# Kernel optimization log

Measured on AMD Instinct MI355X. Metric: run time of the kernel, lower is better.

## Reference

```python
import jax, jax.numpy as jnp
import numpy as np

N_NODES = 8192
N_EDGES = 262144
N_REL = 8
NUM_CLASSES = 151
EMB = 256
BOX = 1024
HID = 512
OUT = 256
N_TASKS = 2


def setup_inputs() -> dict:
    key = jax.random.key(0)
    ks = jax.random.split(key, 20)
    w = lambda k, shape: jax.random.normal(k, shape, dtype=jnp.float32) * 0.02
    return {
        "box_features": jax.random.normal(ks[0], (N_NODES, BOX), dtype=jnp.float32),
        "pred_labels": jax.random.randint(ks[1], (N_NODES,), 0, NUM_CLASSES),
        "edge_index": jax.random.randint(ks[2], (2, N_EDGES), 0, N_NODES),
        "edge_type": jax.random.randint(ks[3], (N_EDGES,), 0, N_REL),
        "nodes_per_graph": 128,
        "emb_table": w(ks[4], (NUM_CLASSES, EMB)),
        "W_lin": w(ks[5], (BOX + EMB, HID)),
        "b_lin": jnp.zeros((HID,), jnp.float32),
        "rel_W1": w(ks[6], (N_REL, HID, HID)),
        "root_W1": w(ks[7], (HID, HID)),
        "b1": jnp.zeros((HID,), jnp.float32),
        "rel_W2": w(ks[8], (N_REL, HID, OUT)),
        "root_W2": w(ks[9], (HID, OUT)),
        "b2": jnp.zeros((OUT,), jnp.float32),
        "Wc1": w(ks[10], (OUT, OUT)),
        "bc1": jnp.zeros((OUT,), jnp.float32),
        "Wc2": w(ks[11], (OUT, N_TASKS)),
        "bc2": jnp.zeros((N_TASKS,), jnp.float32),
    }


def rgcn_conv(x, src, dst, etype, rel_W, root_W, b):
    """PyG RGCNConv: per-relation mean aggregation + root weight + bias."""
    R, _, out_dim = rel_W.shape
    N = x.shape[0]
    transformed = jnp.einsum('ni,rio->rno', x, rel_W)      # [R, N, out]
    msg = transformed[etype, src]                           # [E, out] gather per edge
    seg = etype * N + dst                                   # (relation, dst) segment id
    sums = jax.ops.segment_sum(msg, seg, num_segments=R * N)
    cnt = jax.ops.segment_sum(jnp.ones((msg.shape[0],), x.dtype), seg, num_segments=R * N)
    mean = sums / jnp.maximum(cnt, 1.0)[:, None]
    agg = mean.reshape(R, N, out_dim).sum(0)                # sum over relations
    return agg + x @ root_W + b


def reference(box_features, pred_labels, edge_index, edge_type, nodes_per_graph,
              emb_table, W_lin, b_lin, rel_W1, root_W1, b1, rel_W2, root_W2, b2,
              Wc1, bc1, Wc2, bc2):
    src, dst = edge_index[0], edge_index[1]
    # obj embedding + concat with box features
    x = jnp.concatenate([box_features, emb_table[pred_labels]], axis=-1)  # [N, 1280]
    x = x @ W_lin + b_lin                                                  # [N, 512]
    x = jax.nn.relu(rgcn_conv(x, src, dst, edge_type, rel_W1, root_W1, b1))
    x = rgcn_conv(x, src, dst, edge_type, rel_W2, root_W2, b2)             # [N, 256]
    # mean graph pooling over equal-size graphs
    B = x.shape[0] // nodes_per_graph
    pooled = x.reshape(B, nodes_per_graph, -1).mean(axis=1)                # [B, 256]
    # classifier (dropout is identity in eval)
    y_logits = (pooled @ Wc1 + bc1) @ Wc2 + bc2                            # [B, n_tasks]
    y_prob = jax.nn.softmax(y_logits, axis=-1)
    return y_logits, y_prob
```

## Files before the change

kernel.cpp:

```cpp
#include <hip/hip_runtime.h>
#include <cstdint>

#define NNODES 8192
#define NEDGES 262144
#define NRELS  8
#define EMBD   256
#define BOXD   1024
#define HIDD   512
#define OUTD   256
#define NSEG   (NRELS * NNODES)
#define K0DIM  (BOXD + EMBD)
#define KSDIM  (NRELS * HIDD + HIDD)

using bf16x8 = __attribute__((ext_vector_type(8))) short;
using f32x4  = __attribute__((ext_vector_type(4))) float;
using us4    = __attribute__((ext_vector_type(4))) unsigned short;

__device__ __forceinline__ unsigned short f2b(float f) {
    union { float f; uint32_t u; } v; v.f = f;
    uint32_t r = v.u + 0x7FFFu + ((v.u >> 16) & 1u);
    return (unsigned short)(r >> 16);
}

__device__ __forceinline__ us4 cvt4(f32x4 v) {
    us4 u;
    u[0] = f2b(v[0]); u[1] = f2b(v[1]); u[2] = f2b(v[2]); u[3] = f2b(v[3]);
    return u;
}

__device__ __forceinline__ float b2f_lo(uint32_t w) {
    union { uint32_t u; float f; } v; v.u = w << 16; return v.f;
}
__device__ __forceinline__ float b2f_hi(uint32_t w) {
    union { uint32_t u; float f; } v; v.u = w & 0xffff0000u; return v.f;
}

__global__ void k_build_x0(const float* __restrict__ box, const int* __restrict__ labels,
                           const float* __restrict__ emb, unsigned short* __restrict__ X0) {
    int n = blockIdx.x;
    int lab = labels[n];
    const f32x4* b = (const f32x4*)(box + (size_t)n * BOXD);
    const f32x4* e = (const f32x4*)(emb + (size_t)lab * EMBD);
    us4* o = (us4*)(X0 + (size_t)n * K0DIM);
    for (int j = threadIdx.x; j < K0DIM / 4; j += 256) {
        f32x4 v = (j < BOXD / 4) ? b[j] : e[j - BOXD / 4];
        o[j] = cvt4(v);
    }
}

__global__ void k_transpose(const float* __restrict__ src, unsigned short* __restrict__ dst,
                            int No, int ldDst, int kOff) {
    __shared__ float t[32][33];
    int kt = blockIdx.x * 32, ot = blockIdx.y * 32;
    int tx = threadIdx.x & 31, ty = threadIdx.x >> 5;
#pragma unroll
    for (int i = 0; i < 4; i++) {
        int k = kt + ty + i * 8;
        t[ty + i * 8][tx] = src[(size_t)k * No + ot + tx];
    }
    __syncthreads();
#pragma unroll
    for (int i = 0; i < 4; i++) {
        int o = ot + ty + i * 8;
        dst[(size_t)o * ldDst + kOff + kt + tx] = f2b(t[tx][ty + i * 8]);
    }
}

__global__ void k_hist(const int* __restrict__ etype, const int* __restrict__ edst,
                       int* __restrict__ cnt) {
    int e = blockIdx.x * 256 + threadIdx.x;
    if (e >= NEDGES) return;
    atomicAdd(&cnt[etype[e] * NNODES + edst[e]], 1);
}

__global__ void k_scan(const int* __restrict__ cnt, int* __restrict__ segstart) {
    __shared__ int part[256];
    __shared__ int pre[257];
    int t = threadIdx.x;
    int base = t * 256;
    int s = 0;
    for (int i = 0; i < 256; i++) s += cnt[base + i];
    part[t] = s;
    __syncthreads();
    if (t == 0) {
        int a = 0;
        for (int i = 0; i < 256; i++) { pre[i] = a; a += part[i]; }
        pre[256] = a;
    }
    __syncthreads();
    int a = pre[t];
    for (int i = 0; i < 256; i++) { segstart[base + i] = a; a += cnt[base + i]; }
    if (t == 255) segstart[NSEG] = a;
}

__global__ void k_scatter(const int* __restrict__ etype, const int* __restrict__ esrc,
                          const int* __restrict__ edst, const int* __restrict__ segstart,
                          int* __restrict__ cursor, int* __restrict__ esorted) {
    int e = blockIdx.x * 256 + threadIdx.x;
    if (e >= NEDGES) return;
    int key = etype[e] * NNODES + edst[e];
    int pos = atomicAdd(&cursor[key], 1);
    esorted[segstart[key] + pos] = esrc[e];
}

__global__ void k_inv(const int* __restrict__ cnt, float* __restrict__ inv) {
    int s = blockIdx.x * 256 + threadIdx.x;
    if (s >= NSEG) return;
    int c = cnt[s];
    inv[s] = 1.0f / (float)(c > 0 ? c : 1);
}

__global__ __launch_bounds__(256) void k_aggregate(
        const unsigned short* __restrict__ x, const int* __restrict__ segstart,
        const int* __restrict__ esorted, const float* __restrict__ inv,
        unsigned short* __restrict__ Xin) {
    int seg = blockIdx.x * 4 + (threadIdx.x >> 6);
    int lane = threadIdx.x & 63;
    int r = seg >> 13;
    int dstn = seg & (NNODES - 1);
    float a[8] = {0, 0, 0, 0, 0, 0, 0, 0};
    float b[8] = {0, 0, 0, 0, 0, 0, 0, 0};
    int s0 = segstart[seg], s1 = segstart[seg + 1];
    int t = s0;
    for (; t + 2 <= s1; t += 2) {
        uint4 v0 = *(const uint4*)(x + (size_t)esorted[t] * HIDD + lane * 8);
        uint4 v1 = *(const uint4*)(x + (size_t)esorted[t + 1] * HIDD + lane * 8);
        a[0] += b2f_lo(v0.x); a[1] += b2f_hi(v0.x);
        a[2] += b2f_lo(v0.y); a[3] += b2f_hi(v0.y);
        a[4] += b2f_lo(v0.z); a[5] += b2f_hi(v0.z);
        a[6] += b2f_lo(v0.w); a[7] += b2f_hi(v0.w);
        b[0] += b2f_lo(v1.x); b[1] += b2f_hi(v1.x);
        b[2] += b2f_lo(v1.y); b[3] += b2f_hi(v1.y);
        b[4] += b2f_lo(v1.z); b[5] += b2f_hi(v1.z);
        b[6] += b2f_lo(v1.w); b[7] += b2f_hi(v1.w);
    }
    if (t < s1) {
        uint4 v0 = *(const uint4*)(x + (size_t)esorted[t] * HIDD + lane * 8);
        a[0] += b2f_lo(v0.x); a[1] += b2f_hi(v0.x);
        a[2] += b2f_lo(v0.y); a[3] += b2f_hi(v0.y);
        a[4] += b2f_lo(v0.z); a[5] += b2f_hi(v0.z);
        a[6] += b2f_lo(v0.w); a[7] += b2f_hi(v0.w);
    }
    float iv = inv[seg];
#pragma unroll
    for (int j = 0; j < 8; j++) a[j] = (a[j] + b[j]) * iv;
    uint4 u;
    u.x = (uint32_t)f2b(a[0]) | ((uint32_t)f2b(a[1]) << 16);
    u.y = (uint32_t)f2b(a[2]) | ((uint32_t)f2b(a[3]) << 16);
    u.z = (uint32_t)f2b(a[4]) | ((uint32_t)f2b(a[5]) << 16);
    u.w = (uint32_t)f2b(a[6]) | ((uint32_t)f2b(a[7]) << 16);
    *(uint4*)(Xin + (size_t)dstn * KSDIM + r * HIDD + lane * 8) = u;
}

__global__ __launch_bounds__(512, 4) void k_gemm(
        const unsigned short* __restrict__ A,
        const unsigned short* __restrict__ Bt,
        float* __restrict__ P,
        int M, int N, int K, int Kc) {
    __shared__ unsigned short As[2][128 * 64];
    __shared__ unsigned short Bs[2][128 * 64];
    const int tid = threadIdx.x;
    const int lane = tid & 63, wid = tid >> 6;
    const int tiles_m = M >> 7;
    const int tm = blockIdx.x % tiles_m, tn = blockIdx.x / tiles_m;
    const int m0 = tm << 7, n0 = tn << 7;
    const int wr = wid >> 2, wc = wid & 3;
    const int k0 = blockIdx.y * Kc;

    f32x4 acc[4][2];
#pragma unroll
    for (int i = 0; i < 4; i++)
#pragma unroll
        for (int j = 0; j < 2; j++) acc[i][j] = (f32x4){0.f, 0.f, 0.f, 0.f};

    const int rowg = tid >> 3;
    const int srcc = (tid & 7) ^ (rowg & 7);
    const unsigned short* gA = A  + (size_t)(m0 + rowg) * K + k0 + srcc * 8;
    const unsigned short* gB = Bt + (size_t)(n0 + rowg) * K + k0 + srcc * 8;
    const int ldsbase = wid * 512;

    auto stage = [&](int bsel, int kt) {
#pragma unroll
        for (int i = 0; i < 2; ++i) {
            __builtin_amdgcn_global_load_lds(
                (const __attribute__((address_space(1))) void*)(gA + kt + i * 64 * K),
                (__attribute__((address_space(3))) void*)&As[bsel][i * 4096 + ldsbase], 16, 0, 0);
            __builtin_amdgcn_global_load_lds(
                (const __attribute__((address_space(1))) void*)(gB + kt + i * 64 * K),
                (__attribute__((address_space(3))) void*)&Bs[bsel][i * 4096 + ldsbase], 16, 0, 0);
        }
    };

    const int arow = wr * 64 + (lane & 15);
    const int brow = wc * 32 + (lane & 15);
    const int l7 = lane & 7;
    const int c0 = lane >> 4;

    const int nt = Kc >> 6;
    int cur = 0;
    stage(0, 0);
    asm volatile("s_waitcnt vmcnt(0)" ::: "memory");
    __builtin_amdgcn_s_barrier();

    for (int t = 0; t < nt; ++t) {
        if (t + 1 < nt) stage(cur ^ 1, (t + 1) * 64);
#pragma unroll
        for (int s4 = 0; s4 < 2; ++s4) {
            const int slot = (c0 + s4 * 4) ^ l7;
            bf16x8 af[4], bfr[2];
#pragma unroll
            for (int m = 0; m < 4; m++)
                af[m] = *(const bf16x8*)&As[cur][(arow + m * 16) * 64 + slot * 8];
#pragma unroll
            for (int n = 0; n < 2; n++)
                bfr[n] = *(const bf16x8*)&Bs[cur][(brow + n * 16) * 64 + slot * 8];
#pragma unroll
            for (int m = 0; m < 4; m++)
#pragma unroll
                for (int n = 0; n < 2; n++)
                    acc[m][n] = __builtin_amdgcn_mfma_f32_16x16x32_bf16(af[m], bfr[n], acc[m][n], 0, 0, 0);
        }
        if (t + 1 < nt) {
            asm volatile("s_waitcnt vmcnt(0)" ::: "memory");
            __builtin_amdgcn_s_barrier();
            cur ^= 1;
        }
    }

    float* Pout = P + (size_t)blockIdx.y * M * N;
    const int crow0 = m0 + wr * 64 + (lane >> 4) * 4;
    const int ccol0 = n0 + wc * 32 + (lane & 15);
#pragma unroll
    for (int n = 0; n < 2; n++) {
        int col = ccol0 + n * 16;
#pragma unroll
        for (int m = 0; m < 4; m++)
#pragma unroll
            for (int r = 0; r < 4; r++)
                Pout[(size_t)(crow0 + m * 16 + r) * N + col] = acc[m][n][r];
    }
}

template <int RELU>
__global__ void k_reduce_bf(const float* __restrict__ P, const float* __restrict__ bias,
                            unsigned short* __restrict__ xbf, unsigned short* __restrict__ Xin,
                            int MN) {
    int idx = (blockIdx.x * 256 + threadIdx.x) * 4;
    f32x4 v = *(const f32x4*)&P[idx];
    v += *(const f32x4*)&P[(size_t)MN + idx];
    v += *(const f32x4*)&bias[idx & 511];
    if (RELU) {
#pragma unroll
        for (int j = 0; j < 4; j++) v[j] = fmaxf(v[j], 0.f);
    }
    us4 u = cvt4(v);
    *(us4*)&xbf[idx] = u;
    int row = idx >> 9, col = idx & 511;
    *(us4*)&Xin[(size_t)row * KSDIM + NRELS * HIDD + col] = u;
}

__global__ void k_reduce4(const float* P, const float* __restrict__ bias,
                          float* out, int MN, int N) {
    int idx = (blockIdx.x * 256 + threadIdx.x) * 4;
    f32x4 v = *(const f32x4*)&P[idx];
#pragma unroll
    for (int s = 1; s < 4; s++) v += *(const f32x4*)&P[(size_t)s * MN + idx];
    v += *(const f32x4*)&bias[idx & (N - 1)];
    *(f32x4*)&out[idx] = v;
}

__global__ void k_pool(const float* __restrict__ x3, float* __restrict__ pooled) {
    int b = blockIdx.x, o = threadIdx.x;
    float s = 0.f;
    for (int i = 0; i < 128; i++) s += x3[(size_t)(b * 128 + i) * OUTD + o];
    pooled[b * OUTD + o] = s * (1.0f / 128.0f);
}

__global__ void k_classifier(const float* __restrict__ pooled, const float* __restrict__ Wc1,
                             const float* __restrict__ bc1, const float* __restrict__ Wc2,
                             const float* __restrict__ bc2, float* __restrict__ out) {
    __shared__ float h[256];
    __shared__ float lg[2];
    int b = blockIdx.x, o = threadIdx.x;
    const float* p = pooled + b * 256;
    float s = bc1[o];
    for (int i = 0; i < 256; i++) s += p[i] * Wc1[i * 256 + o];
    h[o] = s;
    __syncthreads();
    if (o < 2) {
        float t = bc2[o];
        for (int i = 0; i < 256; i++) t += h[i] * Wc2[i * 2 + o];
        lg[o] = t;
        out[b * 2 + o] = t;
    }
    __syncthreads();
    if (o == 0) {
        float m = fmaxf(lg[0], lg[1]);
        float e0 = expf(lg[0] - m), e1 = expf(lg[1] - m);
        float inv = 1.0f / (e0 + e1);
        out[128 + b * 2 + 0] = e0 * inv;
        out[128 + b * 2 + 1] = e1 * inv;
    }
}

extern "C" void kernel_launch(void* const* d_in, const int* in_sizes, int n_in,
                              void* d_out, int out_size, void* d_ws, size_t ws_size,
                              hipStream_t stream) {
    const float* box     = (const float*)d_in[0];
    const int*   labels  = (const int*)d_in[1];
    const int*   eidx    = (const int*)d_in[2];
    const int*   etype   = (const int*)d_in[3];
    const float* emb     = (const float*)d_in[5];
    const float* W_lin   = (const float*)d_in[6];
    const float* b_lin   = (const float*)d_in[7];
    const float* rel_W1  = (const float*)d_in[8];
    const float* root_W1 = (const float*)d_in[9];
    const float* b1      = (const float*)d_in[10];
    const float* rel_W2  = (const float*)d_in[11];
    const float* root_W2 = (const float*)d_in[12];
    const float* b2      = (const float*)d_in[13];
    const float* Wc1     = (const float*)d_in[14];
    const float* bc1     = (const float*)d_in[15];
    const float* Wc2     = (const float*)d_in[16];
    const float* bc2     = (const float*)d_in[17];
    const int* esrc = eidx;
    const int* edst = eidx + NEDGES;

    char* ws = (char*)d_ws;
    size_t off = 0;
    auto alloc = [&](size_t bytes) -> char* {
        char* p = ws + off;
        off += (bytes + 255) & ~(size_t)255;
        return p;
    };
    float* Pp = (float*)alloc((size_t)2 * NNODES * HIDD * 4);
    float* x3 = Pp;
    unsigned short* X0   = (unsigned short*)alloc((size_t)NNODES * K0DIM * 2);
    unsigned short* xbf  = X0;
    unsigned short* W0t  = (unsigned short*)alloc((size_t)HIDD * K0DIM * 2);
    unsigned short* W1t  = (unsigned short*)alloc((size_t)HIDD * KSDIM * 2);
    unsigned short* W2t  = (unsigned short*)alloc((size_t)OUTD * KSDIM * 2);
    unsigned short* Xin  = (unsigned short*)alloc((size_t)NNODES * KSDIM * 2);
    int*   cnt     = (int*)alloc((size_t)NSEG * 4);
    int*   cursor  = (int*)alloc((size_t)NSEG * 4);
    int*   segst   = (int*)alloc((size_t)(NSEG + 1) * 4);
    float* inv     = (float*)alloc((size_t)NSEG * 4);
    int*   esorted = (int*)alloc((size_t)NEDGES * 4);
    float* pooled  = (float*)alloc((size_t)64 * OUTD * 4);
    if (off > ws_size) return;

    float* out = (float*)d_out;

    hipMemsetAsync(cnt, 0, NSEG * 4, stream);
    hipMemsetAsync(cursor, 0, NSEG * 4, stream);
    k_build_x0<<<NNODES, 256, 0, stream>>>(box, labels, emb, X0);
    k_transpose<<<dim3(K0DIM / 32, HIDD / 32), 256, 0, stream>>>(W_lin, W0t, HIDD, K0DIM, 0);
    k_transpose<<<dim3(4096 / 32, HIDD / 32), 256, 0, stream>>>(rel_W1, W1t, HIDD, KSDIM, 0);
    k_transpose<<<dim3(HIDD / 32, HIDD / 32), 256, 0, stream>>>(root_W1, W1t, HIDD, KSDIM, 4096);
    k_transpose<<<dim3(4096 / 32, OUTD / 32), 256, 0, stream>>>(rel_W2, W2t, OUTD, KSDIM, 0);
    k_transpose<<<dim3(HIDD / 32, OUTD / 32), 256, 0, stream>>>(root_W2, W2t, OUTD, KSDIM, 4096);
    k_hist<<<NEDGES / 256, 256, 0, stream>>>(etype, edst, cnt);
    k_scan<<<1, 256, 0, stream>>>(cnt, segst);
    k_scatter<<<NEDGES / 256, 256, 0, stream>>>(etype, esrc, edst, segst, cursor, esorted);
    k_inv<<<NSEG / 256, 256, 0, stream>>>(cnt, inv);

    k_gemm<<<dim3((NNODES / 128) * (HIDD / 128), 2), 512, 0, stream>>>(
        X0, W0t, Pp, NNODES, HIDD, K0DIM, K0DIM / 2);
    k_reduce_bf<0><<<(NNODES * HIDD) / 1024, 256, 0, stream>>>(
        Pp, b_lin, xbf, Xin, NNODES * HIDD);

    k_aggregate<<<NSEG / 4, 256, 0, stream>>>(xbf, segst, esorted, inv, Xin);
    k_gemm<<<dim3((NNODES / 128) * (HIDD / 128), 2), 512, 0, stream>>>(
        Xin, W1t, Pp, NNODES, HIDD, KSDIM, KSDIM / 2);
    k_reduce_bf<1><<<(NNODES * HIDD) / 1024, 256, 0, stream>>>(
        Pp, b1, xbf, Xin, NNODES * HIDD);

    k_aggregate<<<NSEG / 4, 256, 0, stream>>>(xbf, segst, esorted, inv, Xin);
    k_gemm<<<dim3((NNODES / 128) * (OUTD / 128), 4), 512, 0, stream>>>(
        Xin, W2t, Pp, NNODES, OUTD, KSDIM, KSDIM / 4);
    k_reduce4<<<(NNODES * OUTD) / 1024, 256, 0, stream>>>(
        Pp, b2, x3, NNODES * OUTD, OUTD);

    k_pool<<<64, 256, 0, stream>>>(x3, pooled);
    k_classifier<<<64, 256, 0, stream>>>(pooled, Wc1, bc1, Wc2, bc2, out);
}
```

Before: 294.4 us.

## Merge small kernels, widen scan, and reshape GEMM to 4-wave 64x64 warp tiles

Merges the five weight-transpose launches into one, computes inverse segment counts inline in aggregate instead of in a separate kernel, and fuses pooling with the classifier. The two memsets become one, which relies on cnt and cursor being adjacent in the workspace. The scan now runs 1024 threads with a two-level prefix. The GEMM moves from 8 waves with 64x32 warp tiles to 4 waves with 64x64 warp tiles, which doubles per-wave register accumulators and changes occupancy. The goal is fewer launches plus more MFMA reuse per LDS fragment load.

```diff
diff --git a/kernel.cpp b/kernel.cpp
--- a/kernel.cpp
+++ b/kernel.cpp
@@ -48,10 +48,20 @@
     }
 }
 
-__global__ void k_transpose(const float* __restrict__ src, unsigned short* __restrict__ dst,
-                            int No, int ldDst, int kOff) {
+__global__ void k_transpose_all(const float* __restrict__ W_lin, const float* __restrict__ rel_W1,
+                                const float* __restrict__ root_W1, const float* __restrict__ rel_W2,
+                                const float* __restrict__ root_W2,
+                                unsigned short* __restrict__ W0t, unsigned short* __restrict__ W1t,
+                                unsigned short* __restrict__ W2t) {
     __shared__ float t[32][33];
-    int kt = blockIdx.x * 32, ot = blockIdx.y * 32;
+    int bid = blockIdx.x;
+    const float* src; unsigned short* dst; int No, ld, kOff, kb, ob;
+    if (bid < 640)        { int g = bid;        src = W_lin;   dst = W0t; No = 512; ld = K0DIM; kOff = 0;    kb = g % 40;  ob = g / 40; }
+    else if (bid < 2688)  { int g = bid - 640;  src = rel_W1;  dst = W1t; No = 512; ld = KSDIM; kOff = 0;    kb = g % 128; ob = g / 128; }
+    else if (bid < 2944)  { int g = bid - 2688; src = root_W1; dst = W1t; No = 512; ld = KSDIM; kOff = 4096; kb = g % 16;  ob = g / 16; }
+    else if (bid < 3968)  { int g = bid - 2944; src = rel_W2;  dst = W2t; No = 256; ld = KSDIM; kOff = 0;    kb = g % 128; ob = g / 128; }
+    else                  { int g = bid - 3968; src = root_W2; dst = W2t; No = 256; ld = KSDIM; kOff = 4096; kb = g % 16;  ob = g / 16; }
+    int kt = kb * 32, ot = ob * 32;
     int tx = threadIdx.x & 31, ty = threadIdx.x >> 5;
 #pragma unroll
     for (int i = 0; i < 4; i++) {
@@ -62,7 +72,7 @@
 #pragma unroll
     for (int i = 0; i < 4; i++) {
         int o = ot + ty + i * 8;
-        dst[(size_t)o * ldDst + kOff + kt + tx] = f2b(t[tx][ty + i * 8]);
+        dst[(size_t)o * ld + kOff + kt + tx] = f2b(t[tx][ty + i * 8]);
     }
 }
 
@@ -73,24 +83,32 @@
     atomicAdd(&cnt[etype[e] * NNODES + edst[e]], 1);
 }
 
-__global__ void k_scan(const int* __restrict__ cnt, int* __restrict__ segstart) {
-    __shared__ int part[256];
-    __shared__ int pre[257];
+__global__ __launch_bounds__(1024) void k_scan(const int* __restrict__ cnt,
+                                               int* __restrict__ segstart) {
+    __shared__ int part[1024];
+    __shared__ int sup[16];
+    __shared__ int supx[16];
     int t = threadIdx.x;
-    int base = t * 256;
+    int base = t * 64;
     int s = 0;
-    for (int i = 0; i < 256; i++) s += cnt[base + i];
+    for (int i = 0; i < 64; i++) s += cnt[base + i];
     part[t] = s;
+    __syncthreads();
+    if (t < 16) {
+        int a = 0;
+        for (int i = 0; i < 64; i++) a += part[t * 64 + i];
+        sup[t] = a;
+    }
     __syncthreads();
     if (t == 0) {
         int a = 0;
-        for (int i = 0; i < 256; i++) { pre[i] = a; a += part[i]; }
-        pre[256] = a;
-    }
-    __syncthreads();
-    int a = pre[t];
-    for (int i = 0; i < 256; i++) { segstart[base + i] = a; a += cnt[base + i]; }
-    if (t == 255) segstart[NSEG] = a;
+        for (int i = 0; i < 16; i++) { supx[i] = a; a += sup[i]; }
+    }
+    __syncthreads();
+    int a = supx[t >> 6];
+    for (int i = (t & ~63); i < t; i++) a += part[i];
+    for (int i = 0; i < 64; i++) { segstart[base + i] = a; a += cnt[base + i]; }
+    if (t == 1023) segstart[NSEG] = a;
 }
 
 __global__ void k_scatter(const int* __restrict__ etype, const int* __restrict__ esrc,
@@ -103,17 +121,9 @@
     esorted[segstart[key] + pos] = esrc[e];
 }
 
-__global__ void k_inv(const int* __restrict__ cnt, float* __restrict__ inv) {
-    int s = blockIdx.x * 256 + threadIdx.x;
-    if (s >= NSEG) return;
-    int c = cnt[s];
-    inv[s] = 1.0f / (float)(c > 0 ? c : 1);
-}
-
 __global__ __launch_bounds__(256) void k_aggregate(
         const unsigned short* __restrict__ x, const int* __restrict__ segstart,
-        const int* __restrict__ esorted, const float* __restrict__ inv,
-        unsigned short* __restrict__ Xin) {
+        const int* __restrict__ esorted, unsigned short* __restrict__ Xin) {
     int seg = blockIdx.x * 4 + (threadIdx.x >> 6);
     int lane = threadIdx.x & 63;
     int r = seg >> 13;
@@ -141,7 +151,7 @@
         a[4] += b2f_lo(v0.z); a[5] += b2f_hi(v0.z);
         a[6] += b2f_lo(v0.w); a[7] += b2f_hi(v0.w);
     }
-    float iv = inv[seg];
+    float iv = (s1 > s0) ? (1.0f / (float)(s1 - s0)) : 1.0f;
 #pragma unroll
     for (int j = 0; j < 8; j++) a[j] = (a[j] + b[j]) * iv;
     uint4 u;
@@ -152,7 +162,7 @@
     *(uint4*)(Xin + (size_t)dstn * KSDIM + r * HIDD + lane * 8) = u;
 }
 
-__global__ __launch_bounds__(512, 4) void k_gemm(
+__global__ __launch_bounds__(256, 2) void k_gemm(
         const unsigned short* __restrict__ A,
         const unsigned short* __restrict__ Bt,
         float* __restrict__ P,
@@ -164,14 +174,14 @@
     const int tiles_m = M >> 7;
     const int tm = blockIdx.x % tiles_m, tn = blockIdx.x / tiles_m;
     const int m0 = tm << 7, n0 = tn << 7;
-    const int wr = wid >> 2, wc = wid & 3;
+    const int wr = wid >> 1, wc = wid & 1;
     const int k0 = blockIdx.y * Kc;
 
-    f32x4 acc[4][2];
+    f32x4 acc[4][4];
 #pragma unroll
     for (int i = 0; i < 4; i++)
 #pragma unroll
-        for (int j = 0; j < 2; j++) acc[i][j] = (f32x4){0.f, 0.f, 0.f, 0.f};
+        for (int j = 0; j < 4; j++) acc[i][j] = (f32x4){0.f, 0.f, 0.f, 0.f};
 
     const int rowg = tid >> 3;
     const int srcc = (tid & 7) ^ (rowg & 7);
@@ -181,18 +191,18 @@
 
     auto stage = [&](int bsel, int kt) {
 #pragma unroll
-        for (int i = 0; i < 2; ++i) {
+        for (int i = 0; i < 4; ++i) {
             __builtin_amdgcn_global_load_lds(
-                (const __attribute__((address_space(1))) void*)(gA + kt + i * 64 * K),
-                (__attribute__((address_space(3))) void*)&As[bsel][i * 4096 + ldsbase], 16, 0, 0);
+                (const __attribute__((address_space(1))) void*)(gA + kt + i * 32 * K),
+                (__attribute__((address_space(3))) void*)&As[bsel][i * 2048 + ldsbase], 16, 0, 0);
             __builtin_amdgcn_global_load_lds(
-                (const __attribute__((address_space(1))) void*)(gB + kt + i * 64 * K),
-                (__attribute__((address_space(3))) void*)&Bs[bsel][i * 4096 + ldsbase], 16, 0, 0);
+                (const __attribute__((address_space(1))) void*)(gB + kt + i * 32 * K),
+                (__attribute__((address_space(3))) void*)&Bs[bsel][i * 2048 + ldsbase], 16, 0, 0);
         }
     };
 
     const int arow = wr * 64 + (lane & 15);
-    const int brow = wc * 32 + (lane & 15);
+    const int brow = wc * 64 + (lane & 15);
     const int l7 = lane & 7;
     const int c0 = lane >> 4;
 
@@ -207,17 +217,17 @@
 #pragma unroll
         for (int s4 = 0; s4 < 2; ++s4) {
             const int slot = (c0 + s4 * 4) ^ l7;
-            bf16x8 af[4], bfr[2];
+            bf16x8 af[4], bfr[4];
 #pragma unroll
             for (int m = 0; m < 4; m++)
                 af[m] = *(const bf16x8*)&As[cur][(arow + m * 16) * 64 + slot * 8];
 #pragma unroll
-            for (int n = 0; n < 2; n++)
+            for (int n = 0; n < 4; n++)
                 bfr[n] = *(const bf16x8*)&Bs[cur][(brow + n * 16) * 64 + slot * 8];
 #pragma unroll
             for (int m = 0; m < 4; m++)
 #pragma unroll
-                for (int n = 0; n < 2; n++)
+                for (int n = 0; n < 4; n++)
                     acc[m][n] = __builtin_amdgcn_mfma_f32_16x16x32_bf16(af[m], bfr[n], acc[m][n], 0, 0, 0);
         }
         if (t + 1 < nt) {
@@ -229,9 +239,9 @@
 
     float* Pout = P + (size_t)blockIdx.y * M * N;
     const int crow0 = m0 + wr * 64 + (lane >> 4) * 4;
-    const int ccol0 = n0 + wc * 32 + (lane & 15);
-#pragma unroll
-    for (int n = 0; n < 2; n++) {
+    const int ccol0 = n0 + wc * 64 + (lane & 15);
+#pragma unroll
+    for (int n = 0; n < 4; n++) {
         int col = ccol0 + n * 16;
 #pragma unroll
         for (int m = 0; m < 4; m++)
@@ -269,23 +279,20 @@
     *(f32x4*)&out[idx] = v;
 }
 
-__global__ void k_pool(const float* __restrict__ x3, float* __restrict__ pooled) {
+__global__ void k_poolclass(const float* __restrict__ x3, const float* __restrict__ Wc1,
+                            const float* __restrict__ bc1, const float* __restrict__ Wc2,
+                            const float* __restrict__ bc2, float* __restrict__ out) {
+    __shared__ float p[256];
+    __shared__ float h[256];
+    __shared__ float lg[2];
     int b = blockIdx.x, o = threadIdx.x;
     float s = 0.f;
     for (int i = 0; i < 128; i++) s += x3[(size_t)(b * 128 + i) * OUTD + o];
-    pooled[b * OUTD + o] = s * (1.0f / 128.0f);
-}
-
-__global__ void k_classifier(const float* __restrict__ pooled, const float* __restrict__ Wc1,
-                             const float* __restrict__ bc1, const float* __restrict__ Wc2,
-                             const float* __restrict__ bc2, float* __restrict__ out) {
-    __shared__ float h[256];
-    __shared__ float lg[2];
-    int b = blockIdx.x, o = threadIdx.x;
-    const float* p = pooled + b * 256;
-    float s = bc1[o];
-    for (int i = 0; i < 256; i++) s += p[i] * Wc1[i * 256 + o];
-    h[o] = s;
+    p[o] = s * (1.0f / 128.0f);
+    __syncthreads();
+    float s1 = bc1[o];
+    for (int i = 0; i < 256; i++) s1 += p[i] * Wc1[i * 256 + o];
+    h[o] = s1;
     __syncthreads();
     if (o < 2) {
         float t = bc2[o];
@@ -344,43 +351,35 @@
     int*   cnt     = (int*)alloc((size_t)NSEG * 4);
     int*   cursor  = (int*)alloc((size_t)NSEG * 4);
     int*   segst   = (int*)alloc((size_t)(NSEG + 1) * 4);
-    float* inv     = (float*)alloc((size_t)NSEG * 4);
     int*   esorted = (int*)alloc((size_t)NEDGES * 4);
-    float* pooled  = (float*)alloc((size_t)64 * OUTD * 4);
     if (off > ws_size) return;
 
     float* out = (float*)d_out;
 
-    hipMemsetAsync(cnt, 0, NSEG * 4, stream);
-    hipMemsetAsync(cursor, 0, NSEG * 4, stream);
+    hipMemsetAsync(cnt, 0, (size_t)2 * NSEG * 4, stream);
     k_build_x0<<<NNODES, 256, 0, stream>>>(box, labels, emb, X0);
-    k_transpose<<<dim3(K0DIM / 32, HIDD / 32), 256, 0, stream>>>(W_lin, W0t, HIDD, K0DIM, 0);
-    k_transpose<<<dim3(4096 / 32, HIDD / 32), 256, 0, stream>>>(rel_W1, W1t, HIDD, KSDIM, 0);
-    k_transpose<<<dim3(HIDD / 32, HIDD / 32), 256, 0, stream>>>(root_W1, W1t, HIDD, KSDIM, 4096);
-    k_transpose<<<dim3(4096 / 32, OUTD / 32), 256, 0, stream>>>(rel_W2, W2t, OUTD, KSDIM, 0);
-    k_transpose<<<dim3(HIDD / 32, OUTD / 32), 256, 0, stream>>>(root_W2, W2t, OUTD, KSDIM, 4096);
+    k_transpose_all<<<4096, 256, 0, stream>>>(W_lin, rel_W1, root_W1, rel_W2, root_W2,
+                                              W0t, W1t, W2t);
     k_hist<<<NEDGES / 256, 256, 0, stream>>>(etype, edst, cnt);
-    k_scan<<<1, 256, 0, stream>>>(cnt, segst);
+    k_scan<<<1, 1024, 0, stream>>>(cnt, segst);
     k_scatter<<<NEDGES / 256, 256, 0, stream>>>(etype, esrc, edst, segst, cursor, esorted);
-    k_inv<<<NSEG / 256, 256, 0, stream>>>(cnt, inv);
-
-    k_gemm<<<dim3((NNODES / 128) * (HIDD / 128), 2), 512, 0, stream>>>(
+
+    k_gemm<<<dim3((NNODES / 128) * (HIDD / 128), 2), 256, 0, stream>>>(
         X0, W0t, Pp, NNODES, HIDD, K0DIM, K0DIM / 2);
     k_reduce_bf<0><<<(NNODES * HIDD) / 1024, 256, 0, stream>>>(
         Pp, b_lin, xbf, Xin, NNODES * HIDD);
 
-    k_aggregate<<<NSEG / 4, 256, 0, stream>>>(xbf, segst, esorted, inv, Xin);
-    k_gemm<<<dim3((NNODES / 128) * (HIDD / 128), 2), 512, 0, stream>>>(
+    k_aggregate<<<NSEG / 4, 256, 0, stream>>>(xbf, segst, esorted, Xin);
+    k_gemm<<<dim3((NNODES / 128) * (HIDD / 128), 2), 256, 0, stream>>>(
         Xin, W1t, Pp, NNODES, HIDD, KSDIM, KSDIM / 2);
     k_reduce_bf<1><<<(NNODES * HIDD) / 1024, 256, 0, stream>>>(
         Pp, b1, xbf, Xin, NNODES * HIDD);
 
-    k_aggregate<<<NSEG / 4, 256, 0, stream>>>(xbf, segst, esorted, inv, Xin);
-    k_gemm<<<dim3((NNODES / 128) * (OUTD / 128), 4), 512, 0, stream>>>(
+    k_aggregate<<<NSEG / 4, 256, 0, stream>>>(xbf, segst, esorted, Xin);
+    k_gemm<<<dim3((NNODES / 128) * (OUTD / 128), 4), 256, 0, stream>>>(
         Xin, W2t, Pp, NNODES, OUTD, KSDIM, KSDIM / 4);
     k_reduce4<<<(NNODES * OUTD) / 1024, 256, 0, stream>>>(
         Pp, b2, x3, NNODES * OUTD, OUTD);
 
-    k_pool<<<64, 256, 0, stream>>>(x3, pooled);
-    k_classifier<<<64, 256, 0, stream>>>(pooled, Wc1, bc1, Wc2, bc2, out);
-}
+    k_poolclass<<<64, 256, 0, stream>>>(x3, Wc1, bc1, Wc2, bc2, out);
+}
```

After: 282.0 us. -4.2%, faster.
